# Optimization experiments

Hardware: AMD Instinct MI355X
Metric: run time of the kernel (lower is better)

The kernel has to match this reference:

```python
import jax, jax.numpy as jnp
import numpy as np

NEG_INF = -jnp.inf


def setup_inputs() -> dict:
    key = jax.random.key(0)
    k1, k2, k3 = jax.random.split(key, 3)
    B, S, D_IN, E = 16, 2048, 1024, 1024
    feats = jax.random.normal(k1, (B * S, D_IN), dtype=jnp.float32)
    masks = (jax.random.uniform(k2, (B * S, 1)) > 0.1).astype(jnp.float32)
    W = jax.random.normal(k3, (D_IN, E), dtype=jnp.float32) * 0.02
    b = jnp.zeros((E,), dtype=jnp.float32)
    return {"feats": feats, "masks": masks, "W": W, "b": b, "num_steps": S}


def reference(feats, masks, W, b, num_steps):
    B = feats.shape[0] // num_steps
    feats = feats.reshape(B, num_steps, feats.shape[-1])          # (B,S,D_in)
    x = jnp.einsum("bsd,de->bse", feats, W) + b                   # feats_proj

    masks_seq = (masks.reshape(B, num_steps, -1) != 0).any(-1)    # (B,S) bool
    masks_f = masks_seq.astype(x.dtype)

    # position ids: cumsum of mask, zeroed where mask == 0
    position_ids = jnp.where(masks_seq, jnp.cumsum(masks_f, axis=1), 0.0)

    # episodic attention mask: episode_start[j] = last k<=j with mask==0 (default 0)
    idx = jnp.arange(num_steps)                                   # (S,)
    start_cand = jnp.where(masks_seq, 0, idx[None, :])            # (B,S)
    ep_start = jax.lax.associative_scan(jnp.maximum, start_cand, axis=1)  # cummax
    allowed = (idx[None, None, :] >= ep_start[:, :, None]) & (
        idx[None, None, :] <= idx[None, :, None]
    )                                                             # (B,S,S)
    attn_mask = jnp.where(allowed, 0.0, NEG_INF).astype(x.dtype)
    return x, position_ids, attn_mask
```

## Files before the change

kernel.cpp:

```cpp
#include <hip/hip_runtime.h>


typedef unsigned int uint;
typedef unsigned short ushort;
typedef __attribute__((ext_vector_type(8))) short bf16x8;
typedef __attribute__((ext_vector_type(4))) float f32x4;
typedef __attribute__((ext_vector_type(8))) ushort u16x8;

__device__ __forceinline__ ushort f2bf_rtn(float x) {
    uint u = __float_as_uint(x);
    uint r = (u + 0x7FFFu + ((u >> 16) & 1u)) >> 16;
    return (ushort)r;
}
__device__ __forceinline__ float bf2f(ushort h) {
    return __uint_as_float((uint)h << 16);
}

__device__ __forceinline__ int lidx(int row, int chunk) {
    return row * 64 + ((chunk ^ (row & 7)) << 3);
}

#define LDS_BARRIER() do {                                        \
    __builtin_amdgcn_sched_barrier(0);                            \
    asm volatile("s_waitcnt lgkmcnt(0)" ::: "memory");            \
    __builtin_amdgcn_s_barrier();                                 \
    __builtin_amdgcn_sched_barrier(0);                            \
} while (0)

__global__ __launch_bounds__(256) void wsplit1_k(
    const float* __restrict__ W, ushort* __restrict__ Wh, int K, int N)
{
    __shared__ float tile[32][33];
    const int n0 = blockIdx.x * 32, k0 = blockIdx.y * 32;
    const int t = threadIdx.x;
    {
        const int nn = t & 31, kk = t >> 5;
        #pragma unroll
        for (int i = 0; i < 4; ++i)
            tile[kk + i * 8][nn] = W[(size_t)(k0 + kk + i * 8) * N + n0 + nn];
    }
    __syncthreads();
    {
        const int kk = t & 31, nn = t >> 5;
        #pragma unroll
        for (int i = 0; i < 4; ++i) {
            float x = tile[kk][nn + i * 8];
            Wh[(size_t)(n0 + nn + i * 8) * K + k0 + kk] = f2bf_rtn(x);
        }
    }
}

__global__ __launch_bounds__(256) void scan_k(
    const float* __restrict__ masks, float* __restrict__ pos_out,
    int* __restrict__ ep_out, int S)
{
    const int b = blockIdx.x, t = threadIdx.x;
    const float* mrow = masks + (size_t)b * S;

    float ls[8]; int lm[8]; bool on8[8];
    float csum = 0.0f; int cmax = 0;
    #pragma unroll
    for (int e = 0; e < 8; ++e) {
        const int j = t * 8 + e;
        const bool on = (mrow[j] != 0.0f);
        on8[e] = on;
        csum += on ? 1.0f : 0.0f;
        if (!on && j > cmax) cmax = j;
        ls[e] = csum;
        lm[e] = cmax;
    }
    __shared__ float ps[256];
    __shared__ int   pm[256];
    ps[t] = csum; pm[t] = cmax;
    __syncthreads();
    for (int off = 1; off < 256; off <<= 1) {
        float s = 0.0f; int m = 0;
        if (t >= off) { s = ps[t - off]; m = pm[t - off]; }
        __syncthreads();
        if (t >= off) { ps[t] += s; pm[t] = (m > pm[t]) ? m : pm[t]; }
        __syncthreads();
    }
    const float esum = (t == 0) ? 0.0f : ps[t - 1];
    const int   emax = (t == 0) ? 0    : pm[t - 1];
    #pragma unroll
    for (int e = 0; e < 8; ++e) {
        const int j = t * 8 + e;
        pos_out[(size_t)b * S + j] = on8[e] ? (esum + ls[e]) : 0.0f;
        const int ep = (lm[e] > emax) ? lm[e] : emax;
        ep_out[(size_t)b * S + j] = ep;
    }
}

__global__ __launch_bounds__(512, 1) void mfma_gemm17_k(
    const float* __restrict__ A, const ushort* __restrict__ Bh,
    const float* __restrict__ bias, float* __restrict__ C,
    const int* __restrict__ ep_ws, float* __restrict__ mask_out,
    int M, int N, int K, int S)
{
    __shared__ ushort Ls[2][256 * 64];

    const int tid  = threadIdx.x;
    const int lane = tid & 63, wv = tid >> 6;
    const int wr   = wv >> 2,  wc = wv & 3;

    const int lin  = blockIdx.x;
    const int wgid = (lin & 7) * 64 + (lin >> 3);
    const int bm = wgid >> 2, bn = wgid & 3;

    const int kc   = tid & 3;
    const int q0   = tid >> 2;
    const int row0 = ((q0 & 3) << 2) | ((q0 >> 2) & 3) | (q0 & ~15);
    const int row1 = row0 | 128;

    const float*  Ag  = A  + (size_t)(bm * 256) * K;
    const ushort* Bhg = Bh + (size_t)(bn * 256) * K;

    float4 a_lo[2], a_hi[2];
    u16x8  b_st[2];

    auto gload = [&](int kt) {
        const int kb = kt * 32 + kc * 8;
        const float* p0 = Ag + (size_t)row0 * K + kb;
        const float* p1 = Ag + (size_t)row1 * K + kb;
        a_lo[0] = *(const float4*)p0;       a_hi[0] = *(const float4*)(p0 + 4);
        a_lo[1] = *(const float4*)p1;       a_hi[1] = *(const float4*)(p1 + 4);
        b_st[0] = *(const u16x8*)(Bhg + (size_t)row0 * K + kb);
        b_st[1] = *(const u16x8*)(Bhg + (size_t)row1 * K + kb);
    };

    auto lwrite = [&](int buf) {
        #pragma unroll
        for (int i = 0; i < 2; ++i) {
            const int row = i ? row1 : row0;
            float xs[8] = {a_lo[i].x, a_lo[i].y, a_lo[i].z, a_lo[i].w,
                           a_hi[i].x, a_hi[i].y, a_hi[i].z, a_hi[i].w};
            u16x8 vh;
            #pragma unroll
            for (int j = 0; j < 8; ++j)
                vh[j] = f2bf_rtn(xs[j]);
            *(u16x8*)&Ls[buf][lidx(row, kc)]     = vh;
            *(u16x8*)&Ls[buf][lidx(row, kc + 4)] = b_st[i];
        }
    };

    f32x4 acc[8][4] = {};

    const int arow0 = wr * 128 + (lane & 15);
    const int brow0 = wc * 64  + (lane & 15);
    const int fq    = lane >> 4;

    const int mrow  = lin * 64 + (tid >> 3);
    const int irow  = mrow & (S - 1);
    const int ep    = ep_ws[mrow];
    const int l8    = tid & 7;
    f32x4* mbase    = (f32x4*)(mask_out + (size_t)mrow * S) + l8;
    const float NEG_BIG = -1.0e30f;

    gload(0);
    lwrite(0);
    __syncthreads();

    int cur = 0;
    const int NT = K / 32;
    for (int kt = 0; kt < NT; ++kt) {
        if (kt + 1 < NT) gload(kt + 1);

        #pragma unroll
        for (int u = 0; u < 2; ++u) {
            const int f  = l8 + 8 * (2 * kt + u);
            const int c0 = f * 4;
            f32x4 v;
            if (c0 >= ep && c0 + 3 <= irow) {
                v = (f32x4){0.0f, 0.0f, 0.0f, 0.0f};
            } else if (c0 + 3 < ep || c0 > irow) {
                v = (f32x4){NEG_BIG, NEG_BIG, NEG_BIG, NEG_BIG};
            } else {
                v[0] = (c0     >= ep && c0     <= irow) ? 0.0f : NEG_BIG;
                v[1] = (c0 + 1 >= ep && c0 + 1 <= irow) ? 0.0f : NEG_BIG;
                v[2] = (c0 + 2 >= ep && c0 + 2 <= irow) ? 0.0f : NEG_BIG;
                v[3] = (c0 + 3 >= ep && c0 + 3 <= irow) ? 0.0f : NEG_BIG;
            }
            __builtin_nontemporal_store(v, mbase + 8 * (2 * kt + u));
        }

        bf16x8 fb[4];
        #pragma unroll
        for (int ni = 0; ni < 4; ++ni)
            fb[ni] = *(const bf16x8*)&Ls[cur][lidx(brow0 + ni * 16, 4 + fq)];
        #pragma unroll
        for (int h = 0; h < 2; ++h) {
            const int rbase = arow0 + h * 64;
            bf16x8 ah[4];
            #pragma unroll
            for (int mi = 0; mi < 4; ++mi)
                ah[mi] = *(const bf16x8*)&Ls[cur][lidx(rbase + mi * 16, fq)];
            #pragma unroll
            for (int mi = 0; mi < 4; ++mi)
                #pragma unroll
                for (int ni = 0; ni < 4; ++ni)
                    acc[h * 4 + mi][ni] = __builtin_amdgcn_mfma_f32_16x16x32_bf16(
                        ah[mi], fb[ni], acc[h * 4 + mi][ni], 0, 0, 0);
        }

        if (kt + 1 < NT) {
            lwrite(cur ^ 1);
            LDS_BARRIER();
            cur ^= 1;
        }
    }

    const int crow = (lane >> 4) * 4;
    #pragma unroll
    for (int ni = 0; ni < 4; ++ni) {
        const int n = bn * 256 + wc * 64 + ni * 16 + (lane & 15);
        const float bv = bias[n];
        #pragma unroll
        for (int mi = 0; mi < 8; ++mi) {
            const int m0 = bm * 256 + wr * 128 + mi * 16 + crow;
            #pragma unroll
            for (int jj = 0; jj < 4; ++jj)
                __builtin_nontemporal_store(acc[mi][ni][jj] + bv,
                                            &C[(size_t)(m0 + jj) * N + n]);
        }
    }
}

#define BM 128
#define BN 128
#define BK 16

__global__ __launch_bounds__(256) void proj_gemm_k(
    const float* __restrict__ A, const float* __restrict__ B,
    const float* __restrict__ bias, float* __restrict__ C,
    int M, int N, int K)
{
    constexpr int LA = BM + 4;
    constexpr int LB = BN + 4;
    __shared__ __align__(16) float As[2][BK][LA];
    __shared__ __align__(16) float Bs[2][BK][LB];

    const int tid = threadIdx.x;
    const int bn  = blockIdx.x;
    const int bm  = blockIdx.y;
    const int ty  = tid >> 4;
    const int tx  = tid & 15;

    const float* Ag = A + (size_t)bm * BM * K;
    const float* Bg = B + (size_t)bn * BN;

    const int fa_r = tid >> 2;
    const int fa_c = (tid & 3) * 4;
    const int fb_k = tid >> 5;
    const int fb_c = (tid & 31) * 4;

    const int NT = K / BK;
    float acc[2][2][4][4] = {};
    float4 a0r, a1r, b0r, b1r;

    auto write_tile = [&](int buf) {
        As[buf][fa_c + 0][fa_r] = a0r.x;
        As[buf][fa_c + 1][fa_r] = a0r.y;
        As[buf][fa_c + 2][fa_r] = a0r.z;
        As[buf][fa_c + 3][fa_r] = a0r.w;
        As[buf][fa_c + 0][fa_r + 64] = a1r.x;
        As[buf][fa_c + 1][fa_r + 64] = a1r.y;
        As[buf][fa_c + 2][fa_r + 64] = a1r.z;
        As[buf][fa_c + 3][fa_r + 64] = a1r.w;
        *(float4*)&Bs[buf][fb_k][fb_c]     = b0r;
        *(float4*)&Bs[buf][fb_k + 8][fb_c] = b1r;
    };
    auto load_tile = [&](int kt) {
        const float* ap = Ag + kt * BK;
        a0r = *(const float4*)(ap + (size_t)fa_r * K + fa_c);
        a1r = *(const float4*)(ap + (size_t)(fa_r + 64) * K + fa_c);
        const float* bp = Bg + (size_t)kt * BK * N;
        b0r = *(const float4*)(bp + (size_t)fb_k * N + fb_c);
        b1r = *(const float4*)(bp + (size_t)(fb_k + 8) * N + fb_c);
    };

    load_tile(0);
    write_tile(0);
    __syncthreads();

    int cur = 0;
    for (int kt = 0; kt < NT; ++kt) {
        if (kt + 1 < NT) load_tile(kt + 1);
        #pragma unroll
        for (int k = 0; k < BK; ++k) {
            float4 x0 = *(const float4*)&As[cur][k][ty * 4];
            float4 x1 = *(const float4*)&As[cur][k][64 + ty * 4];
            float4 y0 = *(const float4*)&Bs[cur][k][tx * 4];
            float4 y1 = *(const float4*)&Bs[cur][k][64 + tx * 4];
            float avv[2][4] = {{x0.x, x0.y, x0.z, x0.w}, {x1.x, x1.y, x1.z, x1.w}};
            float bvv[2][4] = {{y0.x, y0.y, y0.z, y0.w}, {y1.x, y1.y, y1.z, y1.w}};
            #pragma unroll
            for (int mi = 0; mi < 2; ++mi)
                #pragma unroll
                for (int i = 0; i < 4; ++i)
                    #pragma unroll
                    for (int ni = 0; ni < 2; ++ni)
                        #pragma unroll
                        for (int jj = 0; jj < 4; ++jj)
                            acc[mi][ni][i][jj] = fmaf(avv[mi][i], bvv[ni][jj], acc[mi][ni][i][jj]);
        }
        if (kt + 1 < NT) {
            write_tile(cur ^ 1);
            __syncthreads();
            cur ^= 1;
        }
    }

    #pragma unroll
    for (int ni = 0; ni < 2; ++ni) {
        const int n = bn * BN + ni * 64 + tx * 4;
        float4 bv = *(const float4*)&bias[n];
        #pragma unroll
        for (int mi = 0; mi < 2; ++mi) {
            #pragma unroll
            for (int i = 0; i < 4; ++i) {
                const int m = bm * BM + mi * 64 + ty * 4 + i;
                float4 o;
                o.x = acc[mi][ni][i][0] + bv.x;
                o.y = acc[mi][ni][i][1] + bv.y;
                o.z = acc[mi][ni][i][2] + bv.z;
                o.w = acc[mi][ni][i][3] + bv.w;
                *(float4*)(C + (size_t)m * N + n) = o;
            }
        }
    }
}

__global__ __launch_bounds__(256) void episodic_mask_k(
    const float* __restrict__ masks, float* __restrict__ pos_out,
    float* __restrict__ mask_out, int S)
{
    const int i = blockIdx.x;
    const int b = blockIdx.y;
    const int t = threadIdx.x;
    const float* mrow = masks + (size_t)b * S;

    float sum = 0.0f;
    int   mx  = 0;
    for (int j = t; j <= i; j += 256) {
        const bool on = (mrow[j] != 0.0f);
        sum += on ? 1.0f : 0.0f;
        if (!on && j > mx) mx = j;
    }
    #pragma unroll
    for (int off = 32; off > 0; off >>= 1) {
        sum += __shfl_down(sum, off, 64);
        int o = __shfl_down(mx, off, 64);
        mx = (o > mx) ? o : mx;
    }
    __shared__ float wsum[4];
    __shared__ int   wmax[4];
    __shared__ int   s_ep;
    const int wid = t >> 6, lane = t & 63;
    if (lane == 0) { wsum[wid] = sum; wmax[wid] = mx; }
    __syncthreads();
    if (t == 0) {
        float ts = wsum[0] + wsum[1] + wsum[2] + wsum[3];
        int tm = wmax[0];
        tm = (wmax[1] > tm) ? wmax[1] : tm;
        tm = (wmax[2] > tm) ? wmax[2] : tm;
        tm = (wmax[3] > tm) ? wmax[3] : tm;
        s_ep = tm;
        pos_out[(size_t)b * S + i] = (mrow[i] != 0.0f) ? ts : 0.0f;
    }
    __syncthreads();
    const int ep = s_ep;
    const float NEG_BIG = -1.0e30f;
    float4* orow = (float4*)(mask_out + ((size_t)b * S + i) * S);
    const int nf = S >> 2;
    for (int f = t; f < nf; f += 256) {
        const int j0 = f * 4;
        float4 v;
        v.x = (j0     >= ep && j0     <= i) ? 0.0f : NEG_BIG;
        v.y = (j0 + 1 >= ep && j0 + 1 <= i) ? 0.0f : NEG_BIG;
        v.z = (j0 + 2 >= ep && j0 + 2 <= i) ? 0.0f : NEG_BIG;
        v.w = (j0 + 3 >= ep && j0 + 3 <= i) ? 0.0f : NEG_BIG;
        orow[f] = v;
    }
}

extern "C" void kernel_launch(void* const* d_in, const int* in_sizes, int n_in,
                              void* d_out, int out_size, void* d_ws, size_t ws_size,
                              hipStream_t stream)
{
    const float* feats = (const float*)d_in[0];
    const float* masks = (const float*)d_in[1];
    const float* W     = (const float*)d_in[2];
    const float* bias  = (const float*)d_in[3];

    const int M = in_sizes[1];
    const int K = in_sizes[0] / M;
    const int N = in_sizes[3];
    const int S = out_size / M - N - 1;
    const int B = M / S;

    float* x_out    = (float*)d_out;
    float* pos_out  = x_out + (size_t)M * N;
    float* mask_out = pos_out + M;

    const size_t w_w   = (size_t)K * N * sizeof(ushort);
    const size_t w_all = w_w + (size_t)M * sizeof(int);

    if (ws_size >= w_all && S == 2048 && (M % 64) == 0) {
        ushort* Wh = (ushort*)d_ws;
        int*    ep = (int*)(Wh + (size_t)K * N);
        wsplit1_k<<<dim3(N / 32, K / 32), 256, 0, stream>>>(W, Wh, K, N);
        scan_k<<<B, 256, 0, stream>>>(masks, pos_out, ep, S);
        const int nblk = (M / 256) * (N / 256);
        mfma_gemm17_k<<<nblk, 512, 0, stream>>>(
            feats, Wh, bias, x_out, ep, mask_out, M, N, K, S);
    } else {
        proj_gemm_k<<<dim3(N / BN, M / BM), 256, 0, stream>>>(feats, W, bias, x_out, M, N, K);
        episodic_mask_k<<<dim3(S, B), 256, 0, stream>>>(masks, pos_out, mask_out, S);
    }
}
```

Baseline: 147.6 us.

## Double GEMM K-tile to 64 with row-per-thread-pair staging loads

Raises the per-iteration K depth of the fused GEMM+mask kernel from 32 to 64, halving the number of barrier-synchronized main-loop iterations. Global staging changes so each thread pair loads a contiguous 64-element slice of one row (8 float4 plus 4 bf16x8), with a new 128-wide swizzled LDS layout. The mask-store interleave is rescaled to four stores per iteration. It doubles LDS use to 128 KB and the staging registers, which may limit latency hiding or raise register pressure.

Result: slower. 179.6 us (+21.6%).

```diff
diff --git a/kernel.cpp b/kernel.cpp
--- a/kernel.cpp
+++ b/kernel.cpp
@@ -12,12 +12,9 @@
     uint r = (u + 0x7FFFu + ((u >> 16) & 1u)) >> 16;
     return (ushort)r;
 }
-__device__ __forceinline__ float bf2f(ushort h) {
-    return __uint_as_float((uint)h << 16);
-}
-
-__device__ __forceinline__ int lidx(int row, int chunk) {
-    return row * 64 + ((chunk ^ (row & 7)) << 3);
+
+__device__ __forceinline__ int lidx2(int row, int chunk) {
+    return row * 128 + ((chunk ^ (row & 7)) << 3);
 }
 
 #define LDS_BARRIER() do {                                        \
@@ -91,13 +88,13 @@
     }
 }
 
-__global__ __launch_bounds__(512, 1) void mfma_gemm17_k(
+__global__ __launch_bounds__(512, 1) void mfma_gemm18_k(
     const float* __restrict__ A, const ushort* __restrict__ Bh,
     const float* __restrict__ bias, float* __restrict__ C,
     const int* __restrict__ ep_ws, float* __restrict__ mask_out,
     int M, int N, int K, int S)
 {
-    __shared__ ushort Ls[2][256 * 64];
+    __shared__ ushort Ls[2][256 * 128];
 
     const int tid  = threadIdx.x;
     const int lane = tid & 63, wv = tid >> 6;
@@ -107,39 +104,40 @@
     const int wgid = (lin & 7) * 64 + (lin >> 3);
     const int bm = wgid >> 2, bn = wgid & 3;
 
-    const int kc   = tid & 3;
-    const int q0   = tid >> 2;
-    const int row0 = ((q0 & 3) << 2) | ((q0 >> 2) & 3) | (q0 & ~15);
-    const int row1 = row0 | 128;
-
-    const float*  Ag  = A  + (size_t)(bm * 256) * K;
-    const ushort* Bhg = Bh + (size_t)(bn * 256) * K;
-
-    float4 a_lo[2], a_hi[2];
-    u16x8  b_st[2];
+    const int srow = tid >> 1;
+    const int sh   = tid & 1;
+
+    const float*  Ag  = A  + ((size_t)(bm * 256) + srow) * K;
+    const ushort* Bhg = Bh + ((size_t)(bn * 256) + srow) * K;
+
+    float4 a_st[8];
+    u16x8  b_st[4];
 
     auto gload = [&](int kt) {
-        const int kb = kt * 32 + kc * 8;
-        const float* p0 = Ag + (size_t)row0 * K + kb;
-        const float* p1 = Ag + (size_t)row1 * K + kb;
-        a_lo[0] = *(const float4*)p0;       a_hi[0] = *(const float4*)(p0 + 4);
-        a_lo[1] = *(const float4*)p1;       a_hi[1] = *(const float4*)(p1 + 4);
-        b_st[0] = *(const u16x8*)(Bhg + (size_t)row0 * K + kb);
-        b_st[1] = *(const u16x8*)(Bhg + (size_t)row1 * K + kb);
+        const int kb = kt * 64 + sh * 32;
+        const float* p = Ag + kb;
+        #pragma unroll
+        for (int i = 0; i < 8; ++i)
+            a_st[i] = *(const float4*)(p + i * 4);
+        const ushort* q = Bhg + kb;
+        #pragma unroll
+        for (int c = 0; c < 4; ++c)
+            b_st[c] = *(const u16x8*)(q + c * 8);
     };
 
     auto lwrite = [&](int buf) {
         #pragma unroll
-        for (int i = 0; i < 2; ++i) {
-            const int row = i ? row1 : row0;
-            float xs[8] = {a_lo[i].x, a_lo[i].y, a_lo[i].z, a_lo[i].w,
-                           a_hi[i].x, a_hi[i].y, a_hi[i].z, a_hi[i].w};
+        for (int c = 0; c < 4; ++c) {
             u16x8 vh;
+            float xs[8] = {a_st[2 * c].x,     a_st[2 * c].y,
+                           a_st[2 * c].z,     a_st[2 * c].w,
+                           a_st[2 * c + 1].x, a_st[2 * c + 1].y,
+                           a_st[2 * c + 1].z, a_st[2 * c + 1].w};
             #pragma unroll
             for (int j = 0; j < 8; ++j)
                 vh[j] = f2bf_rtn(xs[j]);
-            *(u16x8*)&Ls[buf][lidx(row, kc)]     = vh;
-            *(u16x8*)&Ls[buf][lidx(row, kc + 4)] = b_st[i];
+            *(u16x8*)&Ls[buf][lidx2(srow, sh * 4 + c)]     = vh;
+            *(u16x8*)&Ls[buf][lidx2(srow, 8 + sh * 4 + c)] = b_st[c];
         }
     };
 
@@ -161,13 +159,13 @@
     __syncthreads();
 
     int cur = 0;
-    const int NT = K / 32;
+    const int NT = K / 64;
     for (int kt = 0; kt < NT; ++kt) {
         if (kt + 1 < NT) gload(kt + 1);
 
         #pragma unroll
-        for (int u = 0; u < 2; ++u) {
-            const int f  = l8 + 8 * (2 * kt + u);
+        for (int u = 0; u < 4; ++u) {
+            const int f  = l8 + 8 * (4 * kt + u);
             const int c0 = f * 4;
             f32x4 v;
             if (c0 >= ep && c0 + 3 <= irow) {
@@ -180,26 +178,29 @@
                 v[2] = (c0 + 2 >= ep && c0 + 2 <= irow) ? 0.0f : NEG_BIG;
                 v[3] = (c0 + 3 >= ep && c0 + 3 <= irow) ? 0.0f : NEG_BIG;
             }
-            __builtin_nontemporal_store(v, mbase + 8 * (2 * kt + u));
-        }
-
-        bf16x8 fb[4];
-        #pragma unroll
-        for (int ni = 0; ni < 4; ++ni)
-            fb[ni] = *(const bf16x8*)&Ls[cur][lidx(brow0 + ni * 16, 4 + fq)];
-        #pragma unroll
-        for (int h = 0; h < 2; ++h) {
-            const int rbase = arow0 + h * 64;
-            bf16x8 ah[4];
-            #pragma unroll
-            for (int mi = 0; mi < 4; ++mi)
-                ah[mi] = *(const bf16x8*)&Ls[cur][lidx(rbase + mi * 16, fq)];
-            #pragma unroll
-            for (int mi = 0; mi < 4; ++mi)
+            __builtin_nontemporal_store(v, mbase + 8 * (4 * kt + u));
+        }
+
+        #pragma unroll
+        for (int j2 = 0; j2 < 2; ++j2) {
+            bf16x8 fb[4];
+            #pragma unroll
+            for (int ni = 0; ni < 4; ++ni)
+                fb[ni] = *(const bf16x8*)&Ls[cur][lidx2(brow0 + ni * 16, 8 + j2 * 4 + fq)];
+            #pragma unroll
+            for (int h = 0; h < 2; ++h) {
+                const int rbase = arow0 + h * 64;
+                bf16x8 ah[4];
                 #pragma unroll
-                for (int ni = 0; ni < 4; ++ni)
-                    acc[h * 4 + mi][ni] = __builtin_amdgcn_mfma_f32_16x16x32_bf16(
-                        ah[mi], fb[ni], acc[h * 4 + mi][ni], 0, 0, 0);
+                for (int mi = 0; mi < 4; ++mi)
+                    ah[mi] = *(const bf16x8*)&Ls[cur][lidx2(rbase + mi * 16, j2 * 4 + fq)];
+                #pragma unroll
+                for (int mi = 0; mi < 4; ++mi)
+                    #pragma unroll
+                    for (int ni = 0; ni < 4; ++ni)
+                        acc[h * 4 + mi][ni] = __builtin_amdgcn_mfma_f32_16x16x32_bf16(
+                            ah[mi], fb[ni], acc[h * 4 + mi][ni], 0, 0, 0);
+            }
         }
 
         if (kt + 1 < NT) {
@@ -405,13 +406,13 @@
     const size_t w_w   = (size_t)K * N * sizeof(ushort);
     const size_t w_all = w_w + (size_t)M * sizeof(int);
 
-    if (ws_size >= w_all && S == 2048 && (M % 64) == 0) {
+    if (ws_size >= w_all && S == 2048 && (M % 64) == 0 && (K % 64) == 0) {
         ushort* Wh = (ushort*)d_ws;
         int*    ep = (int*)(Wh + (size_t)K * N);
         wsplit1_k<<<dim3(N / 32, K / 32), 256, 0, stream>>>(W, Wh, K, N);
         scan_k<<<B, 256, 0, stream>>>(masks, pos_out, ep, S);
         const int nblk = (M / 256) * (N / 256);
-        mfma_gemm17_k<<<nblk, 512, 0, stream>>>(
+        mfma_gemm18_k<<<nblk, 512, 0, stream>>>(
             feats, Wh, bias, x_out, ep, mask_out, M, N, K, S);
     } else {
         proj_gemm_k<<<dim3(N / BN, M / BM), 256, 0, stream>>>(feats, W, bias, x_out, M, N, K);
```
